# Kernel optimization log

Measured on AMD Instinct MI355X. Metric: run time of the kernel, lower is better.

Reference implementation:

```python
import jax, jax.numpy as jnp
import numpy as np

N_NODES = 100000
N_EDGES = 1600000
IN, HID, OUT = 128, 128, 64


def setup_inputs() -> dict:
    key = jax.random.key(0)
    ks = jax.random.split(key, 12)
    x = jax.random.normal(ks[0], (N_NODES, IN), dtype=jnp.float32)
    src = jax.random.randint(ks[1], (N_EDGES,), 0, N_NODES, dtype=jnp.int32)
    dst = jax.random.randint(ks[2], (N_EDGES,), 0, N_NODES, dtype=jnp.int32)
    def lin(k, fan_in, fan_out):
        s = 1.0 / np.sqrt(fan_in)
        return (jax.random.normal(k, (fan_in, fan_out), dtype=jnp.float32) * s)
    dims = [(IN, HID), (HID, HID), (HID, OUT)]
    params = {}
    for l, (fi, fo) in enumerate(dims):
        params[f"Wself{l}"] = lin(ks[3 + 3 * l], fi, fo)
        params[f"Wneigh{l}"] = lin(ks[4 + 3 * l], fi, fo)
        params[f"b{l}"] = jnp.zeros((fo,), dtype=jnp.float32)
    return {"x": x, "src": src, "dst": dst, **params}


def _sage_conv(h, src, dst, inv_deg, Ws, Wn, b):
    # mean aggregation over in-neighbors: segment-sum of gathered src feats / degree
    agg = jax.ops.segment_sum(h[src], dst, num_segments=N_NODES) * inv_deg
    return h @ Ws + agg @ Wn + b


def reference(x, src, dst, Wself0, Wneigh0, b0, Wself1, Wneigh1, b1, Wself2, Wneigh2, b2):
    deg = jax.ops.segment_sum(jnp.ones((N_EDGES,), jnp.float32), dst, num_segments=N_NODES)
    inv_deg = (1.0 / jnp.maximum(deg, 1.0))[:, None]  # zero-degree nodes get zero agg
    h = jax.nn.relu(_sage_conv(x, src, dst, inv_deg, Wself0, Wneigh0, b0))
    h = jax.nn.relu(_sage_conv(h, src, dst, inv_deg, Wself1, Wneigh1, b1))
    h = _sage_conv(h, src, dst, inv_deg, Wself2, Wneigh2, b2)
    return h
```

## Files before the change

### kernel.cpp

```cpp
#include <hip/hip_runtime.h>
#include <hip/hip_bf16.h>

#define N_NODES 100000
#define N_EDGES 1600000
#define BSHIFT 8
#define NB 391
#define BCAP 8192

typedef __attribute__((ext_vector_type(8))) short short8;
typedef __attribute__((ext_vector_type(4))) float f32x4;
typedef unsigned short ushort;
typedef unsigned int uint;

__device__ __forceinline__ ushort f2bf(float f) {
    uint u = __float_as_uint(f);
    uint r = (u + 0x7fffu + ((u >> 16) & 1u)) >> 16;
    return (ushort)r;
}
__device__ __forceinline__ float bflo(uint v) { return __uint_as_float(v << 16); }
__device__ __forceinline__ float bfhi(uint v) { return __uint_as_float(v & 0xffff0000u); }


#define CAST_BLK 6250
#define PREP_BLK (CAST_BLK + 128 + 128 + 64)

__global__ __launch_bounds__(256) void fusedA_kernel(const int* __restrict__ src,
                                                     const int* __restrict__ dst,
                                                     uint* __restrict__ packed,
                                                     int* __restrict__ bucket_cnt, int E,
                                                     const float* __restrict__ x,
                                                     ushort* __restrict__ xb,
                                                     const float* __restrict__ Ws0,
                                                     const float* __restrict__ Wn0,
                                                     const float* __restrict__ Ws1,
                                                     const float* __restrict__ Wn1,
                                                     const float* __restrict__ Ws2,
                                                     const float* __restrict__ Wn2,
                                                     ushort* __restrict__ BT0,
                                                     ushort* __restrict__ BT1,
                                                     ushort* __restrict__ BT2) {
    __shared__ int cnt4[4][NB];
    __shared__ int cur4[4][NB];
    int tid = threadIdx.x;
    if (blockIdx.x < NB) {
        constexpr int PER = 16;
        int w = tid >> 6;
        for (int i = tid; i < 4 * NB; i += 256) ((int*)cnt4)[i] = 0;
        __syncthreads();
        int base = blockIdx.x * (256 * PER);
        int d[PER], s[PER];
#pragma unroll
        for (int i = 0; i < PER; i++) {
            int e = base + tid + i * 256;
            if (e < E) {
                d[i] = dst[e];
                s[i] = src[e];
                atomicAdd(&cnt4[w][d[i] >> BSHIFT], 1);
            } else {
                d[i] = -1;
            }
        }
        __syncthreads();
        for (int i = tid; i < NB; i += 256) {
            int c0 = cnt4[0][i], c1 = cnt4[1][i], c2 = cnt4[2][i], c3 = cnt4[3][i];
            int b0 = atomicAdd(&bucket_cnt[i], c0 + c1 + c2 + c3);
            cur4[0][i] = b0;
            cur4[1][i] = b0 + c0;
            cur4[2][i] = b0 + c0 + c1;
            cur4[3][i] = b0 + c0 + c1 + c2;
        }
        __syncthreads();
#pragma unroll
        for (int i = 0; i < PER; i++) {
            if (d[i] >= 0) {
                int b = d[i] >> BSHIFT;
                int p = atomicAdd(&cur4[w][b], 1);
                packed[(size_t)b * BCAP + p] = ((uint)(d[i] & 255) << 17) | (uint)s[i];
            }
        }
        return;
    }
    int blk = blockIdx.x - NB;
    if (blk < CAST_BLK) {
        long n8 = (long)N_NODES * 128 / 8;
        long g = (long)blk * 256 + tid;
        if (g >= n8) return;
        const float4* x4 = (const float4*)x;
        float4 a = x4[g * 2], b = x4[g * 2 + 1];
        uint4 o;
        o.x = (uint)f2bf(a.x) | ((uint)f2bf(a.y) << 16);
        o.y = (uint)f2bf(a.z) | ((uint)f2bf(a.w) << 16);
        o.z = (uint)f2bf(b.x) | ((uint)f2bf(b.y) << 16);
        o.w = (uint)f2bf(b.z) | ((uint)f2bf(b.w) << 16);
        ((uint4*)xb)[g] = o;
        return;
    }
    int idx = (blk - CAST_BLK) * 256 + tid;
    if (idx < 128 * 256) {
        int n = idx >> 8, k = idx & 255;
        float v = (k < 128) ? Ws0[k * 128 + n] : Wn0[(k - 128) * 128 + n];
        BT0[idx] = f2bf(v);
    } else if (idx < 2 * 128 * 256) {
        idx -= 128 * 256;
        int n = idx >> 8, k = idx & 255;
        float v = (k < 128) ? Ws1[k * 128 + n] : Wn1[(k - 128) * 128 + n];
        BT1[idx] = f2bf(v);
    } else if (idx < 2 * 128 * 256 + 128 * 128) {
        idx -= 2 * 128 * 256;
        int n = idx >> 7, k = idx & 127;
        float v = (n < 64) ? Ws2[k * 64 + n] : Wn2[k * 64 + (n - 64)];
        BT2[idx] = f2bf(v);
    }
}


#define KE 20

__global__ __launch_bounds__(256) void partB_kernel(const uint* __restrict__ packed,
                                                    const int* __restrict__ bucket_cnt,
                                                    int* __restrict__ row_ptr,
                                                    float* __restrict__ inv_deg,
                                                    int* __restrict__ col, int N, int E) {
    __shared__ int deg[256];
    __shared__ int cur[256];
    __shared__ int psum[256];
    __shared__ int sofs;
    int b = blockIdx.x, tid = threadIdx.x;
    int cnt = bucket_cnt[b];
    {
        int part = 0;
        for (int i = tid; i < b; i += 256) part += bucket_cnt[i];
        psum[tid] = part;
        __syncthreads();
        for (int off = 128; off > 0; off >>= 1) {
            if (tid < off) psum[tid] += psum[tid + off];
            __syncthreads();
        }
        if (tid == 0) sofs = psum[0];
        __syncthreads();
    }
    int bofs = sofs;
    const uint* pk = packed + (size_t)b * BCAP;
    deg[tid] = 0;
    __syncthreads();
    uint w[KE];
#pragma unroll
    for (int j = 0; j < KE; j++) {
        int ee = tid + j * 256;
        if (ee < cnt) {
            w[j] = pk[ee];
            atomicAdd(&deg[w[j] >> 17], 1);
        }
    }
    for (int ee = tid + KE * 256; ee < cnt; ee += 256)
        atomicAdd(&deg[pk[ee] >> 17], 1);
    __syncthreads();
    int d0 = deg[tid];
    psum[tid] = d0;
    __syncthreads();
    for (int off = 1; off < 256; off <<= 1) {
        int x = psum[tid];
        int y = (tid >= off) ? psum[tid - off] : 0;
        __syncthreads();
        psum[tid] = x + y;
        __syncthreads();
    }
    int excl = psum[tid] - d0;
    cur[tid] = excl;
    int g = (b << BSHIFT) + tid;
    if (g < N) {
        row_ptr[g] = bofs + excl;
        inv_deg[g] = 1.0f / (float)(d0 > 1 ? d0 : 1);
    }
    if (b == 0 && tid == 0) row_ptr[N] = E;
    __syncthreads();
#pragma unroll
    for (int j = 0; j < KE; j++) {
        int ee = tid + j * 256;
        if (ee < cnt) {
            int p = atomicAdd(&cur[w[j] >> 17], 1);
            col[bofs + p] = (int)(w[j] & 0x1FFFFu);
        }
    }
    for (int ee = tid + KE * 256; ee < cnt; ee += 256) {
        uint ww = pk[ee];
        int p = atomicAdd(&cur[ww >> 17], 1);
        col[bofs + p] = (int)(ww & 0x1FFFFu);
    }
}


__global__ __launch_bounds__(256) void agg_kernel(const ushort* __restrict__ hb,
                                                  const int* __restrict__ row_ptr,
                                                  const int* __restrict__ col,
                                                  const float* __restrict__ inv_deg,
                                                  ushort* __restrict__ aggb, int n) {
    int node = (int)((blockIdx.x * blockDim.x + threadIdx.x) >> 6);
    int lane = threadIdx.x & 63;
    if (node >= n) return;
    int quad = lane >> 4;
    int sub = lane & 15;
    const char* hbase = (const char*)hb;
    int beg = row_ptr[node], end = row_ptr[node + 1];
    float acc[8];
#pragma unroll
    for (int j = 0; j < 8; j++) acc[j] = 0.f;
    int suboff = sub * 16;
    for (int e0 = beg; e0 < end; e0 += 16) {
        int rem = end - e0;
        int idxv[4];
        float msk[4];
#pragma unroll
        for (int j = 0; j < 4; j++) {
            int i = quad + 4 * j;
            msk[j] = (i < rem) ? 1.f : 0.f;
            idxv[j] = col[e0 + ((i < rem) ? i : 0)];
        }
        uint4 v[4];
#pragma unroll
        for (int j = 0; j < 4; j++)
            v[j] = *(const uint4*)(hbase + (((uint)idxv[j] << 8) + suboff));
#pragma unroll
        for (int j = 0; j < 4; j++) {
            acc[0] += bflo(v[j].x) * msk[j]; acc[1] += bfhi(v[j].x) * msk[j];
            acc[2] += bflo(v[j].y) * msk[j]; acc[3] += bfhi(v[j].y) * msk[j];
            acc[4] += bflo(v[j].z) * msk[j]; acc[5] += bfhi(v[j].z) * msk[j];
            acc[6] += bflo(v[j].w) * msk[j]; acc[7] += bfhi(v[j].w) * msk[j];
        }
    }
#pragma unroll
    for (int j = 0; j < 8; j++) {
        acc[j] += __shfl_xor(acc[j], 16);
        acc[j] += __shfl_xor(acc[j], 32);
    }
    if (quad == 0) {
        float inv = inv_deg[node];
        uint4 o;
        o.x = (uint)f2bf(acc[0] * inv) | ((uint)f2bf(acc[1] * inv) << 16);
        o.y = (uint)f2bf(acc[2] * inv) | ((uint)f2bf(acc[3] * inv) << 16);
        o.z = (uint)f2bf(acc[4] * inv) | ((uint)f2bf(acc[5] * inv) << 16);
        o.w = (uint)f2bf(acc[6] * inv) | ((uint)f2bf(acc[7] * inv) << 16);
        *(uint4*)((char*)aggb + (size_t)node * 256 + suboff) = o;
    }
}


template <int FOUT, bool RELU>
__global__ __launch_bounds__(256) void mfma_gemm(const ushort* __restrict__ hb,
                                                 const ushort* __restrict__ aggb,
                                                 const ushort* __restrict__ BTb,
                                                 const float* __restrict__ bias,
                                                 ushort* __restrict__ outp, int nNodes) {
    constexpr int NT = FOUT / 16;
    constexpr int BSTR = 40;
    __shared__ ushort BT[FOUT * BSTR];
    int tid = threadIdx.x;
    int wave = tid >> 6, lane = tid & 63;
    int m = lane & 15, quad = lane >> 4;
    int r0 = blockIdx.x * 128 + wave * 32;
    int arow0 = r0 + m;       if (arow0 >= nNodes) arow0 = nNodes - 1;
    int arow1 = r0 + 16 + m;  if (arow1 >= nNodes) arow1 = nNodes - 1;
    const ushort* hrow0 = hb + (size_t)arow0 * 128;
    const ushort* grow0 = aggb + (size_t)arow0 * 128;
    const ushort* hrow1 = hb + (size_t)arow1 * 128;
    const ushort* grow1 = aggb + (size_t)arow1 * 128;

    f32x4 acc[2][NT];
#pragma unroll
    for (int h = 0; h < 2; h++)
#pragma unroll
        for (int t = 0; t < NT; t++) acc[h][t] = (f32x4){0.f, 0.f, 0.f, 0.f};

#pragma unroll
    for (int kc = 0; kc < 8; kc++) {
        __syncthreads();
        constexpr int UNITS = FOUT * 4;
#pragma unroll
        for (int u0 = 0; u0 < UNITS / 256; u0++) {
            int u = tid + u0 * 256;
            int n = u >> 2, ko = (u & 3) * 8;
            short8 v = *(const short8*)(BTb + n * 256 + kc * 32 + ko);
            *(short8*)(&BT[n * BSTR + ko]) = v;
        }
        __syncthreads();
        int kg = kc * 32 + quad * 8;
        const ushort* ap0 = (kg < 128) ? (hrow0 + kg) : (grow0 + (kg - 128));
        const ushort* ap1 = (kg < 128) ? (hrow1 + kg) : (grow1 + (kg - 128));
        short8 af0 = *(const short8*)ap0;
        short8 af1 = *(const short8*)ap1;
#pragma unroll
        for (int t = 0; t < NT; t++) {
            short8 bfrag = *(const short8*)(&BT[(t * 16 + m) * BSTR + quad * 8]);
            acc[0][t] = __builtin_amdgcn_mfma_f32_16x16x32_bf16(af0, bfrag, acc[0][t], 0, 0, 0);
            acc[1][t] = __builtin_amdgcn_mfma_f32_16x16x32_bf16(af1, bfrag, acc[1][t], 0, 0, 0);
        }
    }

#pragma unroll
    for (int h = 0; h < 2; h++)
#pragma unroll
        for (int reg = 0; reg < 4; reg++) {
            int orow = r0 + h * 16 + quad * 4 + reg;
            if (orow < nNodes) {
#pragma unroll
                for (int t = 0; t < NT; t++) {
                    int j = t * 16 + m;
                    float v = acc[h][t][reg] + bias[j];
                    if (RELU) v = fmaxf(v, 0.f);
                    outp[(size_t)orow * FOUT + j] = f2bf(v);
                }
            }
        }
}


__global__ __launch_bounds__(256) void gemm2a_kernel(const ushort* __restrict__ hb,
                                                     const ushort* __restrict__ BT2b,
                                                     const float* __restrict__ bias,
                                                     float* __restrict__ zs,
                                                     ushort* __restrict__ y2, int nNodes) {
    constexpr int NT = 8;
    constexpr int BSTR = 40;
    __shared__ ushort BT[128 * BSTR];
    int tid = threadIdx.x;
    int wave = tid >> 6, lane = tid & 63;
    int m = lane & 15, quad = lane >> 4;
    int r0 = blockIdx.x * 128 + wave * 32;
    int arow0 = r0 + m;       if (arow0 >= nNodes) arow0 = nNodes - 1;
    int arow1 = r0 + 16 + m;  if (arow1 >= nNodes) arow1 = nNodes - 1;
    const ushort* hrow0 = hb + (size_t)arow0 * 128;
    const ushort* hrow1 = hb + (size_t)arow1 * 128;

    f32x4 acc[2][NT];
#pragma unroll
    for (int h = 0; h < 2; h++)
#pragma unroll
        for (int t = 0; t < NT; t++) acc[h][t] = (f32x4){0.f, 0.f, 0.f, 0.f};

#pragma unroll
    for (int kc = 0; kc < 4; kc++) {
        __syncthreads();
#pragma unroll
        for (int u0 = 0; u0 < 2; u0++) {
            int u = tid + u0 * 256;
            int n = u >> 2, ko = (u & 3) * 8;
            short8 v = *(const short8*)(BT2b + n * 128 + kc * 32 + ko);
            *(short8*)(&BT[n * BSTR + ko]) = v;
        }
        __syncthreads();
        int kg = kc * 32 + quad * 8;
        short8 af0 = *(const short8*)(hrow0 + kg);
        short8 af1 = *(const short8*)(hrow1 + kg);
#pragma unroll
        for (int t = 0; t < NT; t++) {
            short8 bfrag = *(const short8*)(&BT[(t * 16 + m) * BSTR + quad * 8]);
            acc[0][t] = __builtin_amdgcn_mfma_f32_16x16x32_bf16(af0, bfrag, acc[0][t], 0, 0, 0);
            acc[1][t] = __builtin_amdgcn_mfma_f32_16x16x32_bf16(af1, bfrag, acc[1][t], 0, 0, 0);
        }
    }

#pragma unroll
    for (int h = 0; h < 2; h++)
#pragma unroll
        for (int reg = 0; reg < 4; reg++) {
            int orow = r0 + h * 16 + quad * 4 + reg;
            if (orow < nNodes) {
#pragma unroll
                for (int t = 0; t < 4; t++) {
                    int j = t * 16 + m;
                    zs[(size_t)orow * 64 + j] = acc[h][t][reg] + bias[j];
                }
#pragma unroll
                for (int t = 4; t < 8; t++) {
                    int j = (t - 4) * 16 + m;
                    y2[(size_t)orow * 64 + j] = f2bf(acc[h][t][reg]);
                }
            }
        }
}


__global__ __launch_bounds__(256) void agg2_kernel(const ushort* __restrict__ y2,
                                                   const int* __restrict__ row_ptr,
                                                   const int* __restrict__ col,
                                                   const float* __restrict__ inv_deg,
                                                   const float* __restrict__ zs,
                                                   float* __restrict__ out, int n) {
    int node = (int)((blockIdx.x * blockDim.x + threadIdx.x) >> 6);
    int lane = threadIdx.x & 63;
    if (node >= n) return;
    int oct = lane >> 3;
    int sub = lane & 7;
    const char* ybase = (const char*)y2;
    int beg = row_ptr[node], end = row_ptr[node + 1];
    float acc[8];
#pragma unroll
    for (int j = 0; j < 8; j++) acc[j] = 0.f;
    int suboff = sub * 16;
    for (int e0 = beg; e0 < end; e0 += 16) {
        int rem = end - e0;
        int idxv[2];
        float msk[2];
#pragma unroll
        for (int j = 0; j < 2; j++) {
            int i = oct + 8 * j;
            msk[j] = (i < rem) ? 1.f : 0.f;
            idxv[j] = col[e0 + ((i < rem) ? i : 0)];
        }
        uint4 v[2];
#pragma unroll
        for (int j = 0; j < 2; j++)
            v[j] = *(const uint4*)(ybase + (((uint)idxv[j] << 7) + suboff));
#pragma unroll
        for (int j = 0; j < 2; j++) {
            acc[0] += bflo(v[j].x) * msk[j]; acc[1] += bfhi(v[j].x) * msk[j];
            acc[2] += bflo(v[j].y) * msk[j]; acc[3] += bfhi(v[j].y) * msk[j];
            acc[4] += bflo(v[j].z) * msk[j]; acc[5] += bfhi(v[j].z) * msk[j];
            acc[6] += bflo(v[j].w) * msk[j]; acc[7] += bfhi(v[j].w) * msk[j];
        }
    }
#pragma unroll
    for (int j = 0; j < 8; j++) {
        acc[j] += __shfl_xor(acc[j], 8);
        acc[j] += __shfl_xor(acc[j], 16);
        acc[j] += __shfl_xor(acc[j], 32);
    }
    if (oct == 0) {
        float inv = inv_deg[node];
        const float4* z = (const float4*)(zs + (size_t)node * 64 + sub * 8);
        float4 z0 = z[0], z1 = z[1];
        float4 o0, o1;
        o0.x = z0.x + acc[0] * inv; o0.y = z0.y + acc[1] * inv;
        o0.z = z0.z + acc[2] * inv; o0.w = z0.w + acc[3] * inv;
        o1.x = z1.x + acc[4] * inv; o1.y = z1.y + acc[5] * inv;
        o1.z = z1.z + acc[6] * inv; o1.w = z1.w + acc[7] * inv;
        float4* op = (float4*)(out + (size_t)node * 64 + sub * 8);
        op[0] = o0; op[1] = o1;
    }
}

extern "C" void kernel_launch(void* const* d_in, const int* in_sizes, int n_in,
                              void* d_out, int out_size, void* d_ws, size_t ws_size,
                              hipStream_t stream) {
    const float* x   = (const float*)d_in[0];
    const int* src   = (const int*)d_in[1];
    const int* dst   = (const int*)d_in[2];
    const float* Ws0 = (const float*)d_in[3];
    const float* Wn0 = (const float*)d_in[4];
    const float* b0  = (const float*)d_in[5];
    const float* Ws1 = (const float*)d_in[6];
    const float* Wn1 = (const float*)d_in[7];
    const float* b1  = (const float*)d_in[8];
    const float* Ws2 = (const float*)d_in[9];
    const float* Wn2 = (const float*)d_in[10];
    const float* b2  = (const float*)d_in[11];
    float* out = (float*)d_out;

    const int N = N_NODES, E = N_EDGES;

    char* p = (char*)d_ws;
    auto take = [&](size_t bytes) {
        void* r = (void*)p;
        p += (bytes + 255) & ~(size_t)255;
        return r;
    };
    uint* packed    = (uint*)take((size_t)NB * BCAP * 4);
    int* bucket_cnt = (int*)take((size_t)NB * 4);
    int* row_ptr    = (int*)take((size_t)(N + 1) * 4);
    int* col        = (int*)take((size_t)E * 4);
    float* inv_deg  = (float*)take((size_t)N * 4);
    ushort* xb      = (ushort*)take((size_t)N * 128 * 2);
    ushort* h1b     = (ushort*)take((size_t)N * 128 * 2);
    ushort* aggb    = (ushort*)take((size_t)N * 128 * 2);
    ushort* BT0     = (ushort*)take((size_t)128 * 256 * 2);
    ushort* BT1     = (ushort*)take((size_t)128 * 256 * 2);
    ushort* BT2     = (ushort*)take((size_t)128 * 128 * 2);
    ushort* y2 = (ushort*)packed;
    float* zs = (float*)aggb;

    hipMemsetAsync(bucket_cnt, 0, (size_t)NB * 4, stream);
    fusedA_kernel<<<NB + PREP_BLK, 256, 0, stream>>>(src, dst, packed, bucket_cnt, E,
                                                     x, xb, Ws0, Wn0, Ws1, Wn1, Ws2, Wn2,
                                                     BT0, BT1, BT2);
    partB_kernel<<<NB, 256, 0, stream>>>(packed, bucket_cnt, row_ptr, inv_deg, col, N, E);

    int aggGrid = (int)(((long)N * 64 + 255) / 256);
    int gemmGrid = (N + 127) / 128;

    agg_kernel<<<aggGrid, 256, 0, stream>>>(xb, row_ptr, col, inv_deg, aggb, N);
    mfma_gemm<128, true><<<gemmGrid, 256, 0, stream>>>(xb, aggb, BT0, b0, h1b, N);
    agg_kernel<<<aggGrid, 256, 0, stream>>>(h1b, row_ptr, col, inv_deg, aggb, N);
    mfma_gemm<128, true><<<gemmGrid, 256, 0, stream>>>(h1b, aggb, BT1, b1, xb, N);
    gemm2a_kernel<<<gemmGrid, 256, 0, stream>>>(xb, BT2, b2, zs, y2, N);
    agg2_kernel<<<aggGrid, 256, 0, stream>>>(y2, row_ptr, col, inv_deg, zs, out, N);
}
```

Baseline: 360.9 us.

## Transform-then-aggregate for layers 0 and 1, fuse bias/ReLU into aggregation

Layers 0 and 1 now apply the self and neighbor weights to node features first: one GEMM with K=128 and N=256 writes z = h@Ws + b and y = h@Wn as bf16. The aggregation kernel then gathers y, scales by inverse degree, adds z and applies ReLU, so the separate K=256 GEMM over [h, agg] goes away. The GEMMs also stop staging B in LDS and load weight fragments straight from global memory. The trade-offs are an extra bf16 write and read of z per layer, and bf16 rounding of z before the add.

```diff
diff --git a/kernel.cpp b/kernel.cpp
--- a/kernel.cpp
+++ b/kernel.cpp
@@ -96,17 +96,17 @@
         return;
     }
     int idx = (blk - CAST_BLK) * 256 + tid;
-    if (idx < 128 * 256) {
-        int n = idx >> 8, k = idx & 255;
-        float v = (k < 128) ? Ws0[k * 128 + n] : Wn0[(k - 128) * 128 + n];
+    if (idx < 256 * 128) {
+        int n = idx >> 7, k = idx & 127;
+        float v = (n < 128) ? Ws0[k * 128 + n] : Wn0[k * 128 + (n - 128)];
         BT0[idx] = f2bf(v);
-    } else if (idx < 2 * 128 * 256) {
-        idx -= 128 * 256;
-        int n = idx >> 8, k = idx & 255;
-        float v = (k < 128) ? Ws1[k * 128 + n] : Wn1[(k - 128) * 128 + n];
+    } else if (idx < 2 * 256 * 128) {
+        idx -= 256 * 128;
+        int n = idx >> 7, k = idx & 127;
+        float v = (n < 128) ? Ws1[k * 128 + n] : Wn1[k * 128 + (n - 128)];
         BT1[idx] = f2bf(v);
-    } else if (idx < 2 * 128 * 256 + 128 * 128) {
-        idx -= 2 * 128 * 256;
+    } else if (idx < 2 * 256 * 128 + 128 * 128) {
+        idx -= 2 * 256 * 128;
         int n = idx >> 7, k = idx & 127;
         float v = (n < 64) ? Ws2[k * 64 + n] : Wn2[k * 64 + (n - 64)];
         BT2[idx] = f2bf(v);
@@ -190,17 +190,126 @@
 }
 
 
-__global__ __launch_bounds__(256) void agg_kernel(const ushort* __restrict__ hb,
-                                                  const int* __restrict__ row_ptr,
-                                                  const int* __restrict__ col,
-                                                  const float* __restrict__ inv_deg,
-                                                  ushort* __restrict__ aggb, int n) {
+__global__ __launch_bounds__(256) void g01a_kernel(const ushort* __restrict__ hb,
+                                                   const ushort* __restrict__ BTb,
+                                                   const float* __restrict__ bias,
+                                                   ushort* __restrict__ zout,
+                                                   ushort* __restrict__ yout, int nNodes) {
+    int tid = threadIdx.x;
+    int wave = tid >> 6, lane = tid & 63;
+    int m = lane & 15, quad = lane >> 4;
+    int r0 = blockIdx.x * 128 + wave * 32;
+    int arow0 = r0 + m;       if (arow0 >= nNodes) arow0 = nNodes - 1;
+    int arow1 = r0 + 16 + m;  if (arow1 >= nNodes) arow1 = nNodes - 1;
+    const ushort* h0 = hb + (size_t)arow0 * 128;
+    const ushort* h1 = hb + (size_t)arow1 * 128;
+
+    f32x4 acc[2][16];
+#pragma unroll
+    for (int h = 0; h < 2; h++)
+#pragma unroll
+        for (int t = 0; t < 16; t++) acc[h][t] = (f32x4){0.f, 0.f, 0.f, 0.f};
+
+#pragma unroll
+    for (int kc = 0; kc < 4; kc++) {
+        int kg = kc * 32 + quad * 8;
+        short8 af0 = *(const short8*)(h0 + kg);
+        short8 af1 = *(const short8*)(h1 + kg);
+#pragma unroll
+        for (int t = 0; t < 16; t++) {
+            short8 bfrag = *(const short8*)(BTb + (size_t)(t * 16 + m) * 128 + kg);
+            acc[0][t] = __builtin_amdgcn_mfma_f32_16x16x32_bf16(af0, bfrag, acc[0][t], 0, 0, 0);
+            acc[1][t] = __builtin_amdgcn_mfma_f32_16x16x32_bf16(af1, bfrag, acc[1][t], 0, 0, 0);
+        }
+    }
+
+#pragma unroll
+    for (int h = 0; h < 2; h++)
+#pragma unroll
+        for (int reg = 0; reg < 4; reg++) {
+            int orow = r0 + h * 16 + quad * 4 + reg;
+            if (orow < nNodes) {
+#pragma unroll
+                for (int t = 0; t < 8; t++) {
+                    int j = t * 16 + m;
+                    zout[(size_t)orow * 128 + j] = f2bf(acc[h][t][reg] + bias[j]);
+                }
+#pragma unroll
+                for (int t = 8; t < 16; t++) {
+                    int j = (t - 8) * 16 + m;
+                    yout[(size_t)orow * 128 + j] = f2bf(acc[h][t][reg]);
+                }
+            }
+        }
+}
+
+
+__global__ __launch_bounds__(256) void g2a_kernel(const ushort* __restrict__ hb,
+                                                  const ushort* __restrict__ BT2b,
+                                                  const float* __restrict__ bias,
+                                                  float* __restrict__ zs,
+                                                  ushort* __restrict__ y2, int nNodes) {
+    int tid = threadIdx.x;
+    int wave = tid >> 6, lane = tid & 63;
+    int m = lane & 15, quad = lane >> 4;
+    int r0 = blockIdx.x * 128 + wave * 32;
+    int arow0 = r0 + m;       if (arow0 >= nNodes) arow0 = nNodes - 1;
+    int arow1 = r0 + 16 + m;  if (arow1 >= nNodes) arow1 = nNodes - 1;
+    const ushort* h0 = hb + (size_t)arow0 * 128;
+    const ushort* h1 = hb + (size_t)arow1 * 128;
+
+    f32x4 acc[2][8];
+#pragma unroll
+    for (int h = 0; h < 2; h++)
+#pragma unroll
+        for (int t = 0; t < 8; t++) acc[h][t] = (f32x4){0.f, 0.f, 0.f, 0.f};
+
+#pragma unroll
+    for (int kc = 0; kc < 4; kc++) {
+        int kg = kc * 32 + quad * 8;
+        short8 af0 = *(const short8*)(h0 + kg);
+        short8 af1 = *(const short8*)(h1 + kg);
+#pragma unroll
+        for (int t = 0; t < 8; t++) {
+            short8 bfrag = *(const short8*)(BT2b + (size_t)(t * 16 + m) * 128 + kg);
+            acc[0][t] = __builtin_amdgcn_mfma_f32_16x16x32_bf16(af0, bfrag, acc[0][t], 0, 0, 0);
+            acc[1][t] = __builtin_amdgcn_mfma_f32_16x16x32_bf16(af1, bfrag, acc[1][t], 0, 0, 0);
+        }
+    }
+
+#pragma unroll
+    for (int h = 0; h < 2; h++)
+#pragma unroll
+        for (int reg = 0; reg < 4; reg++) {
+            int orow = r0 + h * 16 + quad * 4 + reg;
+            if (orow < nNodes) {
+#pragma unroll
+                for (int t = 0; t < 4; t++) {
+                    int j = t * 16 + m;
+                    zs[(size_t)orow * 64 + j] = acc[h][t][reg] + bias[j];
+                }
+#pragma unroll
+                for (int t = 4; t < 8; t++) {
+                    int j = (t - 4) * 16 + m;
+                    y2[(size_t)orow * 64 + j] = f2bf(acc[h][t][reg]);
+                }
+            }
+        }
+}
+
+
+__global__ __launch_bounds__(256) void aggb_kernel(const ushort* __restrict__ yb,
+                                                   const int* __restrict__ row_ptr,
+                                                   const int* __restrict__ col,
+                                                   const float* __restrict__ inv_deg,
+                                                   const ushort* __restrict__ zb,
+                                                   ushort* __restrict__ hout, int n) {
     int node = (int)((blockIdx.x * blockDim.x + threadIdx.x) >> 6);
     int lane = threadIdx.x & 63;
     if (node >= n) return;
     int quad = lane >> 4;
     int sub = lane & 15;
-    const char* hbase = (const char*)hb;
+    const char* ybase = (const char*)yb;
     int beg = row_ptr[node], end = row_ptr[node + 1];
     float acc[8];
 #pragma unroll
@@ -219,7 +328,7 @@
         uint4 v[4];
 #pragma unroll
         for (int j = 0; j < 4; j++)
-            v[j] = *(const uint4*)(hbase + (((uint)idxv[j] << 8) + suboff));
+            v[j] = *(const uint4*)(ybase + (((uint)idxv[j] << 8) + suboff));
 #pragma unroll
         for (int j = 0; j < 4; j++) {
             acc[0] += bflo(v[j].x) * msk[j]; acc[1] += bfhi(v[j].x) * msk[j];
@@ -235,157 +344,31 @@
     }
     if (quad == 0) {
         float inv = inv_deg[node];
+        uint4 z = *(const uint4*)((const char*)zb + (size_t)node * 256 + suboff);
+        float r0 = fmaxf(bflo(z.x) + acc[0] * inv, 0.f);
+        float r1 = fmaxf(bfhi(z.x) + acc[1] * inv, 0.f);
+        float r2 = fmaxf(bflo(z.y) + acc[2] * inv, 0.f);
+        float r3 = fmaxf(bfhi(z.y) + acc[3] * inv, 0.f);
+        float r4 = fmaxf(bflo(z.z) + acc[4] * inv, 0.f);
+        float r5 = fmaxf(bfhi(z.z) + acc[5] * inv, 0.f);
+        float r6 = fmaxf(bflo(z.w) + acc[6] * inv, 0.f);
+        float r7 = fmaxf(bfhi(z.w) + acc[7] * inv, 0.f);
         uint4 o;
-        o.x = (uint)f2bf(acc[0] * inv) | ((uint)f2bf(acc[1] * inv) << 16);
-        o.y = (uint)f2bf(acc[2] * inv) | ((uint)f2bf(acc[3] * inv) << 16);
-        o.z = (uint)f2bf(acc[4] * inv) | ((uint)f2bf(acc[5] * inv) << 16);
-        o.w = (uint)f2bf(acc[6] * inv) | ((uint)f2bf(acc[7] * inv) << 16);
-        *(uint4*)((char*)aggb + (size_t)node * 256 + suboff) = o;
-    }
-}
-
-
-template <int FOUT, bool RELU>
-__global__ __launch_bounds__(256) void mfma_gemm(const ushort* __restrict__ hb,
-                                                 const ushort* __restrict__ aggb,
-                                                 const ushort* __restrict__ BTb,
-                                                 const float* __restrict__ bias,
-                                                 ushort* __restrict__ outp, int nNodes) {
-    constexpr int NT = FOUT / 16;
-    constexpr int BSTR = 40;
-    __shared__ ushort BT[FOUT * BSTR];
-    int tid = threadIdx.x;
-    int wave = tid >> 6, lane = tid & 63;
-    int m = lane & 15, quad = lane >> 4;
-    int r0 = blockIdx.x * 128 + wave * 32;
-    int arow0 = r0 + m;       if (arow0 >= nNodes) arow0 = nNodes - 1;
-    int arow1 = r0 + 16 + m;  if (arow1 >= nNodes) arow1 = nNodes - 1;
-    const ushort* hrow0 = hb + (size_t)arow0 * 128;
-    const ushort* grow0 = aggb + (size_t)arow0 * 128;
-    const ushort* hrow1 = hb + (size_t)arow1 * 128;
-    const ushort* grow1 = aggb + (size_t)arow1 * 128;
-
-    f32x4 acc[2][NT];
-#pragma unroll
-    for (int h = 0; h < 2; h++)
-#pragma unroll
-        for (int t = 0; t < NT; t++) acc[h][t] = (f32x4){0.f, 0.f, 0.f, 0.f};
-
-#pragma unroll
-    for (int kc = 0; kc < 8; kc++) {
-        __syncthreads();
-        constexpr int UNITS = FOUT * 4;
-#pragma unroll
-        for (int u0 = 0; u0 < UNITS / 256; u0++) {
-            int u = tid + u0 * 256;
-            int n = u >> 2, ko = (u & 3) * 8;
-            short8 v = *(const short8*)(BTb + n * 256 + kc * 32 + ko);
-            *(short8*)(&BT[n * BSTR + ko]) = v;
-        }
-        __syncthreads();
-        int kg = kc * 32 + quad * 8;
-        const ushort* ap0 = (kg < 128) ? (hrow0 + kg) : (grow0 + (kg - 128));
-        const ushort* ap1 = (kg < 128) ? (hrow1 + kg) : (grow1 + (kg - 128));
-        short8 af0 = *(const short8*)ap0;
-        short8 af1 = *(const short8*)ap1;
-#pragma unroll
-        for (int t = 0; t < NT; t++) {
-            short8 bfrag = *(const short8*)(&BT[(t * 16 + m) * BSTR + quad * 8]);
-            acc[0][t] = __builtin_amdgcn_mfma_f32_16x16x32_bf16(af0, bfrag, acc[0][t], 0, 0, 0);
-            acc[1][t] = __builtin_amdgcn_mfma_f32_16x16x32_bf16(af1, bfrag, acc[1][t], 0, 0, 0);
-        }
-    }
-
-#pragma unroll
-    for (int h = 0; h < 2; h++)
-#pragma unroll
-        for (int reg = 0; reg < 4; reg++) {
-            int orow = r0 + h * 16 + quad * 4 + reg;
-            if (orow < nNodes) {
-#pragma unroll
-                for (int t = 0; t < NT; t++) {
-                    int j = t * 16 + m;
-                    float v = acc[h][t][reg] + bias[j];
-                    if (RELU) v = fmaxf(v, 0.f);
-                    outp[(size_t)orow * FOUT + j] = f2bf(v);
-                }
-            }
-        }
-}
-
-
-__global__ __launch_bounds__(256) void gemm2a_kernel(const ushort* __restrict__ hb,
-                                                     const ushort* __restrict__ BT2b,
-                                                     const float* __restrict__ bias,
-                                                     float* __restrict__ zs,
-                                                     ushort* __restrict__ y2, int nNodes) {
-    constexpr int NT = 8;
-    constexpr int BSTR = 40;
-    __shared__ ushort BT[128 * BSTR];
-    int tid = threadIdx.x;
-    int wave = tid >> 6, lane = tid & 63;
-    int m = lane & 15, quad = lane >> 4;
-    int r0 = blockIdx.x * 128 + wave * 32;
-    int arow0 = r0 + m;       if (arow0 >= nNodes) arow0 = nNodes - 1;
-    int arow1 = r0 + 16 + m;  if (arow1 >= nNodes) arow1 = nNodes - 1;
-    const ushort* hrow0 = hb + (size_t)arow0 * 128;
-    const ushort* hrow1 = hb + (size_t)arow1 * 128;
-
-    f32x4 acc[2][NT];
-#pragma unroll
-    for (int h = 0; h < 2; h++)
-#pragma unroll
-        for (int t = 0; t < NT; t++) acc[h][t] = (f32x4){0.f, 0.f, 0.f, 0.f};
-
-#pragma unroll
-    for (int kc = 0; kc < 4; kc++) {
-        __syncthreads();
-#pragma unroll
-        for (int u0 = 0; u0 < 2; u0++) {
-            int u = tid + u0 * 256;
-            int n = u >> 2, ko = (u & 3) * 8;
-            short8 v = *(const short8*)(BT2b + n * 128 + kc * 32 + ko);
-            *(short8*)(&BT[n * BSTR + ko]) = v;
-        }
-        __syncthreads();
-        int kg = kc * 32 + quad * 8;
-        short8 af0 = *(const short8*)(hrow0 + kg);
-        short8 af1 = *(const short8*)(hrow1 + kg);
-#pragma unroll
-        for (int t = 0; t < NT; t++) {
-            short8 bfrag = *(const short8*)(&BT[(t * 16 + m) * BSTR + quad * 8]);
-            acc[0][t] = __builtin_amdgcn_mfma_f32_16x16x32_bf16(af0, bfrag, acc[0][t], 0, 0, 0);
-            acc[1][t] = __builtin_amdgcn_mfma_f32_16x16x32_bf16(af1, bfrag, acc[1][t], 0, 0, 0);
-        }
-    }
-
-#pragma unroll
-    for (int h = 0; h < 2; h++)
-#pragma unroll
-        for (int reg = 0; reg < 4; reg++) {
-            int orow = r0 + h * 16 + quad * 4 + reg;
-            if (orow < nNodes) {
-#pragma unroll
-                for (int t = 0; t < 4; t++) {
-                    int j = t * 16 + m;
-                    zs[(size_t)orow * 64 + j] = acc[h][t][reg] + bias[j];
-                }
-#pragma unroll
-                for (int t = 4; t < 8; t++) {
-                    int j = (t - 4) * 16 + m;
-                    y2[(size_t)orow * 64 + j] = f2bf(acc[h][t][reg]);
-                }
-            }
-        }
-}
-
-
-__global__ __launch_bounds__(256) void agg2_kernel(const ushort* __restrict__ y2,
-                                                   const int* __restrict__ row_ptr,
-                                                   const int* __restrict__ col,
-                                                   const float* __restrict__ inv_deg,
-                                                   const float* __restrict__ zs,
-                                                   float* __restrict__ out, int n) {
+        o.x = (uint)f2bf(r0) | ((uint)f2bf(r1) << 16);
+        o.y = (uint)f2bf(r2) | ((uint)f2bf(r3) << 16);
+        o.z = (uint)f2bf(r4) | ((uint)f2bf(r5) << 16);
+        o.w = (uint)f2bf(r6) | ((uint)f2bf(r7) << 16);
+        *(uint4*)((char*)hout + (size_t)node * 256 + suboff) = o;
+    }
+}
+
+
+__global__ __launch_bounds__(256) void agg2b_kernel(const ushort* __restrict__ y2,
+                                                    const int* __restrict__ row_ptr,
+                                                    const int* __restrict__ col,
+                                                    const float* __restrict__ inv_deg,
+                                                    const float* __restrict__ zs,
+                                                    float* __restrict__ out, int n) {
     int node = (int)((blockIdx.x * blockDim.x + threadIdx.x) >> 6);
     int lane = threadIdx.x & 63;
     if (node >= n) return;
@@ -471,12 +454,12 @@
     float* inv_deg  = (float*)take((size_t)N * 4);
     ushort* xb      = (ushort*)take((size_t)N * 128 * 2);
     ushort* h1b     = (ushort*)take((size_t)N * 128 * 2);
-    ushort* aggb    = (ushort*)take((size_t)N * 128 * 2);
-    ushort* BT0     = (ushort*)take((size_t)128 * 256 * 2);
-    ushort* BT1     = (ushort*)take((size_t)128 * 256 * 2);
+    ushort* zbuf    = (ushort*)take((size_t)N * 128 * 2);
+    ushort* ybuf    = (ushort*)take((size_t)N * 128 * 2);
+    ushort* BT0     = (ushort*)take((size_t)256 * 128 * 2);
+    ushort* BT1     = (ushort*)take((size_t)256 * 128 * 2);
     ushort* BT2     = (ushort*)take((size_t)128 * 128 * 2);
-    ushort* y2 = (ushort*)packed;
-    float* zs = (float*)aggb;
+    float* zs = (float*)zbuf;
 
     hipMemsetAsync(bucket_cnt, 0, (size_t)NB * 4, stream);
     fusedA_kernel<<<NB + PREP_BLK, 256, 0, stream>>>(src, dst, packed, bucket_cnt, E,
@@ -487,10 +470,10 @@
     int aggGrid = (int)(((long)N * 64 + 255) / 256);
     int gemmGrid = (N + 127) / 128;
 
-    agg_kernel<<<aggGrid, 256, 0, stream>>>(xb, row_ptr, col, inv_deg, aggb, N);
-    mfma_gemm<128, true><<<gemmGrid, 256, 0, stream>>>(xb, aggb, BT0, b0, h1b, N);
-    agg_kernel<<<aggGrid, 256, 0, stream>>>(h1b, row_ptr, col, inv_deg, aggb, N);
-    mfma_gemm<128, true><<<gemmGrid, 256, 0, stream>>>(h1b, aggb, BT1, b1, xb, N);
-    gemm2a_kernel<<<gemmGrid, 256, 0, stream>>>(xb, BT2, b2, zs, y2, N);
-    agg2_kernel<<<aggGrid, 256, 0, stream>>>(y2, row_ptr, col, inv_deg, zs, out, N);
-}
+    g01a_kernel<<<gemmGrid, 256, 0, stream>>>(xb, BT0, b0, zbuf, ybuf, N);
+    aggb_kernel<<<aggGrid, 256, 0, stream>>>(ybuf, row_ptr, col, inv_deg, zbuf, h1b, N);
+    g01a_kernel<<<gemmGrid, 256, 0, stream>>>(h1b, BT1, b1, zbuf, ybuf, N);
+    aggb_kernel<<<aggGrid, 256, 0, stream>>>(ybuf, row_ptr, col, inv_deg, zbuf, xb, N);
+    g2a_kernel<<<gemmGrid, 256, 0, stream>>>(xb, BT2, b2, zs, ybuf, N);
+    agg2b_kernel<<<aggGrid, 256, 0, stream>>>(ybuf, row_ptr, col, inv_deg, zs, out, N);
+}
```

Result: slower. 432.2 us (+19.8%).
